# Kernel tuning notes

Hardware: AMD Instinct MI355X
Metric: run time of the kernel (lower is better)

The kernel has to match this reference:

```python
import jax, jax.numpy as jnp
import numpy as np

B, N, D = 16, 1024, 1152
H = 16; DH = D // H
GH = GW = 32; SY = SX = 2
WS = SY * SX                      # tokens per window
NW = (GH // SY) * (GW // SX)      # 256 windows (one dst each)
NS = NW * (WS - 1)                # 768 src tokens
NUM_PRUNE = int(N * 0.5)          # 512
NOISE_ALPHA = 0.1
SIM_BETA = 1.0


def setup_inputs() -> dict:
    key = jax.random.key(0)
    ks = jax.random.split(key, 8)
    rn = lambda k, s: jax.random.normal(k, s, jnp.float32) * 0.02
    return dict(
        x=jax.random.normal(ks[0], (B, N, D), jnp.float32),
        noise=jax.random.uniform(ks[1], (B, NW, WS), jnp.float32),
        ln1_g=jnp.ones((D,), jnp.float32), ln1_b=jnp.zeros((D,), jnp.float32),
        ln2_g=jnp.ones((D,), jnp.float32), ln2_b=jnp.zeros((D,), jnp.float32),
        w_qkv=rn(ks[2], (D, 3 * D)), b_qkv=jnp.zeros((3 * D,), jnp.float32),
        w_proj=rn(ks[3], (D, D)), b_proj=jnp.zeros((D,), jnp.float32),
        w_fc1=rn(ks[4], (D, 4 * D)), b_fc1=jnp.zeros((4 * D,), jnp.float32),
        w_fc2=rn(ks[5], (4 * D, D)), b_fc2=jnp.zeros((D,), jnp.float32),
    )


def _ln(x, g, b):
    mu = x.mean(-1, keepdims=True)
    var = ((x - mu) ** 2).mean(-1, keepdims=True)
    return (x - mu) * jax.lax.rsqrt(var + 1e-6) * g + b


def _dit_block(x, ln1_g, ln1_b, ln2_g, ln2_b, w_qkv, b_qkv, w_proj, b_proj,
               w_fc1, b_fc1, w_fc2, b_fc2):
    Bq, T, _ = x.shape
    y = _ln(x, ln1_g, ln1_b)
    q, k, v = jnp.split(y @ w_qkv + b_qkv, 3, axis=-1)
    hd = lambda t: t.reshape(Bq, T, H, DH).transpose(0, 2, 1, 3)  # [B,H,T,DH]
    q, k, v = hd(q), hd(k), hd(v)
    att = jax.nn.softmax(jnp.einsum('bhqd,bhkd->bhqk', q, k) * (1.0 / np.sqrt(DH)), axis=-1)
    o = jnp.einsum('bhqk,bhkd->bhqd', att, v).transpose(0, 2, 1, 3).reshape(Bq, T, D)
    x = x + o @ w_proj + b_proj
    y = _ln(x, ln2_g, ln2_b)
    return x + jax.nn.gelu(y @ w_fc1 + b_fc1) @ w_fc2 + b_fc2


def _sito_indices(x, noise):
    # SiTo seed (dst) selection + similarity-based prune index computation.
    xn = x / (jnp.linalg.norm(x, axis=-1, keepdims=True) + 1e-6)  # cosine feats
    grid = jnp.arange(N).reshape(GH, GW)
    win = grid.reshape(GH // SY, SY, GW // SX, SX).transpose(0, 2, 1, 3).reshape(NW, WS)
    xw = xn[:, win]                                   # [B,NW,WS,D]
    mean = xw.mean(2, keepdims=True)
    score = SIM_BETA * (xw * mean).sum(-1) + NOISE_ALPHA * noise  # [B,NW,WS]
    dst_local = jnp.argmax(score, axis=-1)            # [B,NW]
    winb = jnp.broadcast_to(win, (B, NW, WS))
    dst_idx = jnp.take_along_axis(winb, dst_local[..., None], -1)[..., 0]  # [B,NW]
    local = jnp.arange(WS)[None, None]
    keymat = jnp.where(local != dst_local[..., None], local, WS)
    src_local = jnp.sort(keymat, -1)[..., : WS - 1]   # non-dst locals, in order
    src_idx = jnp.take_along_axis(winb, src_local, -1).reshape(B, NS)
    a = jnp.take_along_axis(xn, src_idx[..., None], 1)      # [B,NS,D]
    bf = jnp.take_along_axis(xn, dst_idx[..., None], 1)     # [B,NW,D]
    sim = jnp.einsum('bsd,bnd->bsn', a, bf)                 # [B,NS,NW]
    best = jnp.argmax(sim, -1)                              # most-similar dst
    order = jnp.argsort(-jnp.max(sim, -1), axis=-1)
    pruned_pos = order[:, :NUM_PRUNE]
    kept_pos = order[:, NUM_PRUNE:]
    src_kept = jnp.take_along_axis(src_idx, kept_pos, 1)
    src_pruned = jnp.take_along_axis(src_idx, pruned_pos, 1)
    pruned_best = jnp.take_along_axis(best, pruned_pos, 1)
    return dst_idx, src_kept, src_pruned, pruned_best


def reference(x, noise, ln1_g, ln1_b, ln2_g, ln2_b, w_qkv, b_qkv, w_proj, b_proj,
              w_fc1, b_fc1, w_fc2, b_fc2):
    dst_idx, src_kept, src_pruned, pruned_best = _sito_indices(x, noise)
    keep_idx = jnp.concatenate([dst_idx, src_kept], axis=1)          # [B,Nk]
    xk = jnp.take_along_axis(x, keep_idx[..., None], 1)              # prune_fn
    out = _dit_block(xk, ln1_g, ln1_b, ln2_g, ln2_b, w_qkv, b_qkv,
                     w_proj, b_proj, w_fc1, b_fc1, w_fc2, b_fc2)

    def recover_one(o, di, sk, sp, pb):  # recover_fn: scatter + copy-from-dst
        out_dst, out_src = o[:NW], o[NW:]
        full = jnp.zeros((N, D), o.dtype)
        full = full.at[di].set(out_dst)
        full = full.at[sk].set(out_src)
        return full.at[sp].set(out_dst[pb])

    return jax.vmap(recover_one)(out, dst_idx, src_kept, src_pruned, pruned_best)
```

## Files before the change

### kernel.cpp

```cpp
#include <hip/hip_runtime.h>
#include <hip/hip_bf16.h>

namespace {

constexpr int Dd = 1152;

typedef __attribute__((ext_vector_type(8))) short bf16x8;
typedef __attribute__((ext_vector_type(4))) float f32x4;

__device__ __forceinline__ void gload_lds16(const void* g, void* l) {
  __builtin_amdgcn_global_load_lds(
      (const __attribute__((address_space(1))) void*)g,
      (__attribute__((address_space(3))) void*)l, 16, 0, 0);
}

__device__ __forceinline__ float gelu_f(float x) {
  float x3 = x * x * x;
  float z2 = 1.5957691216057308f * (x + 0.044715f * x3);
  float e = __expf(fminf(z2, 30.0f));
  return x * e / (e + 1.0f);
}

__global__ __launch_bounds__(256) void norm_kernel(const float* __restrict__ x,
    float* __restrict__ inv, __hip_bfloat16* __restrict__ xnh,
    __hip_bfloat16* __restrict__ xnl) {
  int row = blockIdx.x * 4 + (threadIdx.x >> 6);
  int lane = threadIdx.x & 63;
  const float2* xr = (const float2*)(x + (size_t)row * Dd);
  float2 v[9];
  float s = 0.f;
  #pragma unroll
  for (int e = 0; e < 9; ++e) {
    v[e] = xr[lane + 64 * e];
    s += v[e].x * v[e].x + v[e].y * v[e].y;
  }
  #pragma unroll
  for (int m = 1; m < 64; m <<= 1) s += __shfl_xor(s, m);
  float iv = 1.0f / (sqrtf(s) + 1e-6f);
  if (lane == 0) inv[row] = iv;
  ushort2* ph = (ushort2*)(xnh + (size_t)row * Dd);
  ushort2* pl = (ushort2*)(xnl + (size_t)row * Dd);
  #pragma unroll
  for (int e = 0; e < 9; ++e) {
    float ax = v[e].x * iv, ay = v[e].y * iv;
    __hip_bfloat16 hx = __float2bfloat16(ax), hy = __float2bfloat16(ay);
    __hip_bfloat16 lx = __float2bfloat16(ax - __bfloat162float(hx));
    __hip_bfloat16 ly = __float2bfloat16(ay - __bfloat162float(hy));
    ph[lane + 64 * e] = make_ushort2(*(ushort*)&hx, *(ushort*)&hy);
    pl[lane + 64 * e] = make_ushort2(*(ushort*)&lx, *(ushort*)&ly);
  }
}

__global__ __launch_bounds__(256) void window_kernel(const float* __restrict__ x,
    const float* __restrict__ inv, const float* __restrict__ noise,
    int* __restrict__ dsti, int* __restrict__ srci) {
  int gidx = blockIdx.x * 4 + (threadIdx.x >> 6);
  int lane = threadIdx.x & 63;
  int b = gidx >> 8, w = gidx & 255;
  int wy = w >> 4, wx = w & 15;
  int t0 = (wy * 2) * 32 + wx * 2;
  int tk[4] = {t0, t0 + 1, t0 + 32, t0 + 33};
  float iv[4]; const float* xr[4];
  #pragma unroll
  for (int j = 0; j < 4; ++j) {
    iv[j] = inv[b * 1024 + tk[j]];
    xr[j] = x + (size_t)(b * 1024 + tk[j]) * Dd;
  }
  float dot[4] = {0.f, 0.f, 0.f, 0.f};
  for (int d = lane; d < Dd; d += 64) {
    float xn[4], sum = 0.f;
    #pragma unroll
    for (int j = 0; j < 4; ++j) { xn[j] = xr[j][d] * iv[j]; sum += xn[j]; }
    #pragma unroll
    for (int j = 0; j < 4; ++j) dot[j] += xn[j] * sum;
  }
  #pragma unroll
  for (int m = 1; m < 64; m <<= 1)
    #pragma unroll
    for (int j = 0; j < 4; ++j) dot[j] += __shfl_xor(dot[j], m);
  if (lane == 0) {
    float best = -1e30f; int bj = 0;
    #pragma unroll
    for (int j = 0; j < 4; ++j) {
      float sc = 0.25f * dot[j] + 0.1f * noise[(size_t)(b * 256 + w) * 4 + j];
      if (sc > best) { best = sc; bj = j; }
    }
    dsti[b * 256 + w] = tk[bj];
    int m = 0;
    #pragma unroll
    for (int j = 0; j < 4; ++j) if (j != bj) srci[b * 768 + w * 3 + (m++)] = tk[j];
  }
}

__global__ __launch_bounds__(256) void simgemm_kernel(
    const __hip_bfloat16* __restrict__ xnh, const __hip_bfloat16* __restrict__ xnl,
    const int* __restrict__ dsti, const int* __restrict__ srci,
    float* __restrict__ mx, int* __restrict__ best) {
  int b = blockIdx.x / 12;
  int m0 = (blockIdx.x % 12) * 64;
  __shared__ __align__(16) __hip_bfloat16 AsH[2][64 * 32];
  __shared__ __align__(16) __hip_bfloat16 AsL[2][64 * 32];
  __shared__ __align__(16) __hip_bfloat16 BsH[2][256 * 32];
  __shared__ __align__(16) __hip_bfloat16 BsL[2][256 * 32];
  const int tid = threadIdx.x, wid = tid >> 6, lane = tid & 63;
  const int g = lane >> 4, lr = lane & 15;

  const int slotRow = tid >> 2;
  const int colByte = (((tid & 3) ^ ((tid >> 3) & 3)) << 4);
  size_t aRow = (size_t)((b << 10) + srci[b * 768 + m0 + slotRow]) * Dd;
  size_t bRow[4];
  #pragma unroll
  for (int p = 0; p < 4; ++p)
    bRow[p] = (size_t)((b << 10) + dsti[b * 256 + p * 64 + slotRow]) * Dd;
  const char* xh = (const char*)xnh;
  const char* xl = (const char*)xnl;

  auto stage = [&](int buf, int k0) {
    size_t ka = (aRow + k0) * 2 + colByte;
    gload_lds16(xh + ka, (char*)AsH + buf * 4096 + wid * 1024);
    gload_lds16(xl + ka, (char*)AsL + buf * 4096 + wid * 1024);
    #pragma unroll
    for (int p = 0; p < 4; ++p) {
      size_t kb = (bRow[p] + k0) * 2 + colByte;
      gload_lds16(xh + kb, (char*)BsH + buf * 16384 + p * 4096 + wid * 1024);
      gload_lds16(xl + kb, (char*)BsL + buf * 16384 + p * 4096 + wid * 1024);
    }
  };

  f32x4 hh[16], hx[16];
  const f32x4 zf = {0.f, 0.f, 0.f, 0.f};
  #pragma unroll
  for (int nf = 0; nf < 16; ++nf) { hh[nf] = zf; hx[nf] = zf; }

  const int roff = ((g ^ ((lr >> 1) & 3)) << 3);
  stage(0, 0);
  asm volatile("s_waitcnt vmcnt(0)" ::: "memory");
  __syncthreads();
  int buf = 0;
  for (int ks = 0; ks < 36; ++ks) {
    if (ks + 1 < 36) stage(buf ^ 1, (ks + 1) * 32);
    bf16x8 ah = *(const bf16x8*)&AsH[buf][(wid * 16 + lr) * 32 + roff];
    bf16x8 al = *(const bf16x8*)&AsL[buf][(wid * 16 + lr) * 32 + roff];
    #pragma unroll
    for (int nf = 0; nf < 16; ++nf) {
      bf16x8 bh = *(const bf16x8*)&BsH[buf][(nf * 16 + lr) * 32 + roff];
      bf16x8 bl = *(const bf16x8*)&BsL[buf][(nf * 16 + lr) * 32 + roff];
      hh[nf] = __builtin_amdgcn_mfma_f32_16x16x32_bf16(ah, bh, hh[nf], 0, 0, 0);
      hx[nf] = __builtin_amdgcn_mfma_f32_16x16x32_bf16(ah, bl, hx[nf], 0, 0, 0);
      hx[nf] = __builtin_amdgcn_mfma_f32_16x16x32_bf16(al, bh, hx[nf], 0, 0, 0);
    }
    asm volatile("s_waitcnt vmcnt(0)" ::: "memory");
    __syncthreads();
    buf ^= 1;
  }

  #pragma unroll
  for (int j = 0; j < 4; ++j) {
    float bv = -1e30f; int bi = 0;
    #pragma unroll
    for (int nf = 0; nf < 16; ++nf) {
      float v = hh[nf][j] + hx[nf][j];
      if (v > bv) { bv = v; bi = nf * 16 + lr; }
    }
    #pragma unroll
    for (int m = 1; m < 16; m <<= 1) {
      float ov = __shfl_xor(bv, m);
      int oi = __shfl_xor(bi, m);
      if (ov > bv || (ov == bv && oi < bi)) { bv = ov; bi = oi; }
    }
    if (lr == 0) {
      int row = m0 + wid * 16 + g * 4 + j;
      mx[b * 768 + row] = bv;
      best[b * 768 + row] = bi;
    }
  }
}

__global__ __launch_bounds__(256) void rank_kernel(const float* __restrict__ mx,
    const int* __restrict__ best, const int* __restrict__ dsti,
    const int* __restrict__ srci, int* __restrict__ keep, int* __restrict__ srow) {
  int b = blockIdx.x;
  int tid = threadIdx.x;
  __shared__ float smx[768];
  for (int i = tid; i < 768; i += 256) smx[i] = mx[b * 768 + i];
  __syncthreads();
  if (tid < 256) {
    int t = dsti[b * 256 + tid];
    keep[b * 512 + tid] = t;
    srow[b * 1024 + t] = tid;
  }
  for (int i = tid; i < 768; i += 256) {
    float v = smx[i];
    int r = 0;
    for (int s = 0; s < 768; ++s) {
      float u = smx[s];
      r += (u > v) || (u == v && s < i);
    }
    int tok = srci[b * 768 + i];
    if (r >= 512) {
      keep[b * 512 + (r - 256)] = tok;
      srow[b * 1024 + tok] = r - 256;
    } else {
      srow[b * 1024 + tok] = best[b * 768 + i];
    }
  }
}

template<int GATHER>
__global__ __launch_bounds__(256) void ln_kernel(const float* __restrict__ xin,
    const int* __restrict__ keep, const float* __restrict__ gw,
    const float* __restrict__ bw, __hip_bfloat16* __restrict__ yout) {
  int row = blockIdx.x;
  const float* xr;
  if (GATHER) {
    int b = row >> 9, t = row & 511;
    int tok = keep[(b << 9) + t];
    xr = xin + (size_t)((b << 10) + tok) * Dd;
  } else {
    xr = xin + (size_t)row * Dd;
  }
  int tid = threadIdx.x;
  float v[5];
  float s = 0.f, s2 = 0.f;
  #pragma unroll
  for (int e = 0; e < 5; ++e) {
    int i = tid + e * 256;
    float val = (i < Dd) ? xr[i] : 0.f;
    v[e] = val; s += val; s2 += val * val;
  }
  #pragma unroll
  for (int m = 1; m < 64; m <<= 1) { s += __shfl_xor(s, m); s2 += __shfl_xor(s2, m); }
  __shared__ float ps[4], ps2[4];
  int wid = tid >> 6, lane = tid & 63;
  if (lane == 0) { ps[wid] = s; ps2[wid] = s2; }
  __syncthreads();
  s = ps[0] + ps[1] + ps[2] + ps[3];
  s2 = ps2[0] + ps2[1] + ps2[2] + ps2[3];
  constexpr float inv_d = 1.0f / Dd;
  float mu = s * inv_d;
  float var = s2 * inv_d - mu * mu;
  float rstd = rsqrtf(var + 1e-6f);
  __hip_bfloat16* yr = yout + (size_t)row * Dd;
  #pragma unroll
  for (int e = 0; e < 5; ++e) {
    int i = tid + e * 256;
    if (i < Dd) {
      yr[i] = __float2bfloat16((v[e] - mu) * rstd * gw[i] + bw[i]);
    }
  }
}

__global__ __launch_bounds__(256) void wtrans_kernel(const float* __restrict__ w,
    __hip_bfloat16* __restrict__ wT, int K, int N) {
  __shared__ float tile[32][33];
  int nt = N >> 5;
  int tk = blockIdx.x / nt, tn = blockIdx.x % nt;
  int tid = threadIdx.x;
  #pragma unroll
  for (int e = 0; e < 4; ++e) {
    int idx = tid + e * 256;
    int r = idx >> 5, c = idx & 31;
    tile[r][c] = w[(size_t)(tk * 32 + r) * N + tn * 32 + c];
  }
  __syncthreads();
  #pragma unroll
  for (int e = 0; e < 4; ++e) {
    int idx = tid + e * 256;
    int r = idx >> 5, c = idx & 31;
    wT[(size_t)(tn * 32 + r) * K + tk * 32 + c] = __float2bfloat16(tile[c][r]);
  }
}

template<int EPI>
__device__ __forceinline__ void epi_store(void* C, const float* res, int Nd,
                                          size_t row, size_t col, float v) {
  if (EPI == 0) {
    ((__hip_bfloat16*)C)[row * (size_t)Nd + col] = __float2bfloat16(v);
  } else if (EPI == 1) {
    ((float*)C)[row * (size_t)Nd + col] = v + res[row * (size_t)Nd + col];
  } else if (EPI == 2) {
    ((__hip_bfloat16*)C)[row * (size_t)Nd + col] = __float2bfloat16(gelu_f(v));
  }
}

template<int EPI>
__global__ __launch_bounds__(512, 4) void gemm128_kernel(
    const __hip_bfloat16* __restrict__ A, const __hip_bfloat16* __restrict__ BT,
    const float* __restrict__ bias, const float* __restrict__ res,
    const int* __restrict__ keepIdx, const float* __restrict__ xsrc,
    void* __restrict__ C, int Md, int Nd, int NdPad, int Kd) {
  constexpr int BM = 128;
  __shared__ __align__(16) __hip_bfloat16 As[3][BM * 32];
  __shared__ __align__(16) __hip_bfloat16 Bs[3][256 * 32];
  const int nb = NdPad >> 8;
  const int q8 = gridDim.x >> 3;
  const int wg = (blockIdx.x & 7) * q8 + (blockIdx.x >> 3);
  const int bm = wg / nb, bnb = wg % nb;
  const int tid = threadIdx.x, wid = tid >> 6, lane = tid & 63;
  const int g = lane >> 4, lr = lane & 15;
  const int wm = wid >> 2, wn = wid & 3;
  const size_t m0 = (size_t)bm * BM, n0 = (size_t)bnb * 256;

  const int trow = tid >> 2;
  const int scol = (((tid & 3) ^ ((tid >> 3) & 3)) << 3);
  const char* Ab = (const char*)A;
  const char* Bb = (const char*)BT;

  auto stage = [&](int slot, int kt) {
    const size_t kb = ((size_t)kt << 5) + scol;
    gload_lds16(Ab + (((m0 + trow) * (size_t)Kd + kb) << 1),
                (char*)As + slot * 8192 + wid * 1024);
    gload_lds16(Bb + (((n0 + trow) * (size_t)Kd + kb) << 1),
                (char*)Bs + slot * 16384 + wid * 1024);
    gload_lds16(Bb + (((n0 + 128 + trow) * (size_t)Kd + kb) << 1),
                (char*)Bs + slot * 16384 + 8192 + wid * 1024);
  };

  f32x4 acc[4][4];
  const f32x4 zf = {0.f, 0.f, 0.f, 0.f};
  #pragma unroll
  for (int mi = 0; mi < 4; ++mi)
    #pragma unroll
    for (int ni = 0; ni < 4; ++ni) acc[mi][ni] = zf;

  const int nk = Kd >> 5;
  stage(0, 0);
  stage(1, 1);
  asm volatile("s_waitcnt vmcnt(3)" ::: "memory");
  __builtin_amdgcn_s_barrier();

  int cur = 0;
  const int roff = ((g ^ ((lr >> 1) & 3)) << 3);
  for (int kt = 0; kt < nk; ++kt) {
    const __hip_bfloat16* Ac = As[cur];
    const __hip_bfloat16* Bc = Bs[cur];
    bf16x8 af[4], bf[4];
    #pragma unroll
    for (int mi = 0; mi < 4; ++mi)
      af[mi] = *(const bf16x8*)&Ac[(wm * 64 + mi * 16 + lr) * 32 + roff];
    #pragma unroll
    for (int ni = 0; ni < 4; ++ni)
      bf[ni] = *(const bf16x8*)&Bc[(wn * 64 + ni * 16 + lr) * 32 + roff];
    if (kt + 2 < nk) stage(cur == 0 ? 2 : cur - 1, kt + 2);
    __builtin_amdgcn_s_barrier();
    __builtin_amdgcn_s_setprio(1);
    #pragma unroll
    for (int mi = 0; mi < 4; ++mi)
      #pragma unroll
      for (int ni = 0; ni < 4; ++ni)
        acc[mi][ni] = __builtin_amdgcn_mfma_f32_16x16x32_bf16(af[mi], bf[ni], acc[mi][ni], 0, 0, 0);
    __builtin_amdgcn_s_setprio(0);
    if (kt + 2 < nk)      asm volatile("s_waitcnt vmcnt(3)" ::: "memory");
    else if (kt + 1 < nk) asm volatile("s_waitcnt vmcnt(0)" ::: "memory");
    __builtin_amdgcn_s_barrier();
    cur = (cur == 2) ? 0 : cur + 1;
  }

  #pragma unroll
  for (int ni = 0; ni < 4; ++ni) {
    size_t col = n0 + wn * 64 + ni * 16 + lr;
    if (col < (size_t)Nd) {
      float bv = bias[col];
      #pragma unroll
      for (int mi = 0; mi < 4; ++mi) {
        #pragma unroll
        for (int j = 0; j < 4; ++j) {
          size_t row = m0 + wm * 64 + mi * 16 + g * 4 + j;
          float v = acc[mi][ni][j] + bv;
          if (EPI == 3) {
            int b = (int)(row >> 9);
            int tok = keepIdx[row];
            const float* rr = xsrc + ((size_t)(b << 10) + tok) * Dd;
            ((float*)C)[row * (size_t)Nd + col] = v + rr[col];
          } else {
            epi_store<EPI>(C, res, Nd, row, col, v);
          }
        }
      }
    }
  }
}

__global__ __launch_bounds__(256) void vtrans_kernel(const __hip_bfloat16* __restrict__ qkv,
                                                     __hip_bfloat16* __restrict__ vT) {
  int bh = blockIdx.x;
  int b = bh >> 4, h = bh & 15;
  __shared__ __align__(16) __hip_bfloat16 Vl[256 * 72];
  int tid = threadIdx.x;
  const __hip_bfloat16 zb = __float2bfloat16(0.0f);
  for (int half = 0; half < 2; ++half) {
    __syncthreads();
    for (int idx = tid; idx < 256 * 18; idx += 256) {
      int t = idx / 18, c = idx % 18;
      *(ushort4*)&Vl[t * 72 + c * 4] =
          *(const ushort4*)&qkv[((size_t)(b * 512 + half * 256 + t)) * 3456 + 2304 + h * 72 + c * 4];
    }
    __syncthreads();
    for (int idx = tid; idx < 80 * 256; idx += 256) {
      int d = idx >> 8, t = idx & 255;
      vT[((size_t)bh * 80 + d) * 512 + half * 256 + t] = (d < 72) ? Vl[t * 72 + d] : zb;
    }
  }
}

__global__ __launch_bounds__(256) void attn_kernel(const __hip_bfloat16* __restrict__ qkv,
    const __hip_bfloat16* __restrict__ vT, __hip_bfloat16* __restrict__ o) {
  const int blk = blockIdx.x;
  const int qt = blk & 7, bh = blk >> 3;
  const int b = bh >> 4, h = bh & 15;
  __shared__ __align__(16) __hip_bfloat16 Qs[64][96];
  __shared__ __align__(16) __hip_bfloat16 Ks[64][96];
  __shared__ __align__(16) __hip_bfloat16 Vs[80][72];
  __shared__ __align__(16) __hip_bfloat16 Ps[4][16][72];
  const int tid = threadIdx.x, wid = tid >> 6, lane = tid & 63;
  const int g = lane >> 4, lr = lane & 15;
  const __hip_bfloat16 zb = __float2bfloat16(0.0f);

  for (int idx = tid; idx < 64 * 18; idx += 256) {
    int r = idx / 18, c = idx % 18;
    *(ushort4*)&Qs[r][c * 4] =
        *(const ushort4*)&qkv[((size_t)(b * 512 + qt * 64 + r)) * 3456 + h * 72 + c * 4];
  }
  for (int idx = tid; idx < 64 * 24; idx += 256) {
    int r = idx / 24, d = 72 + idx % 24;
    Qs[r][d] = zb; Ks[r][d] = zb;
  }

  f32x4 ov[5];
  const f32x4 zf = {0.f, 0.f, 0.f, 0.f};
  #pragma unroll
  for (int ni = 0; ni < 5; ++ni) ov[ni] = zf;
  float m_[4], l_[4];
  #pragma unroll
  for (int j = 0; j < 4; ++j) { m_[j] = -3.0e38f; l_[j] = 0.f; }
  const float scale = 0.11785113019775793f;

  for (int c = 0; c < 8; ++c) {
    __syncthreads();
    for (int idx = tid; idx < 64 * 18; idx += 256) {
      int r = idx / 18, cc = idx % 18;
      *(ushort4*)&Ks[r][cc * 4] =
          *(const ushort4*)&qkv[((size_t)(b * 512 + c * 64 + r)) * 3456 + 1152 + h * 72 + cc * 4];
    }
    for (int idx = tid; idx < 80 * 8; idx += 256) {
      int d = idx >> 3, t8 = idx & 7;
      *(uint4*)&Vs[d][t8 * 8] =
          *(const uint4*)&vT[((size_t)bh * 80 + d) * 512 + c * 64 + t8 * 8];
    }
    __syncthreads();

    f32x4 sf[4];
    #pragma unroll
    for (int nf = 0; nf < 4; ++nf) sf[nf] = zf;
    #pragma unroll
    for (int ks = 0; ks < 3; ++ks) {
      bf16x8 qa = *(const bf16x8*)&Qs[wid * 16 + lr][ks * 32 + g * 8];
      #pragma unroll
      for (int nf = 0; nf < 4; ++nf) {
        bf16x8 kb = *(const bf16x8*)&Ks[nf * 16 + lr][ks * 32 + g * 8];
        sf[nf] = __builtin_amdgcn_mfma_f32_16x16x32_bf16(qa, kb, sf[nf], 0, 0, 0);
      }
    }

    float cm[4];
    #pragma unroll
    for (int j = 0; j < 4; ++j)
      cm[j] = fmaxf(fmaxf(sf[0][j], sf[1][j]), fmaxf(sf[2][j], sf[3][j])) * scale;
    #pragma unroll
    for (int mm = 1; mm < 16; mm <<= 1)
      #pragma unroll
      for (int j = 0; j < 4; ++j) cm[j] = fmaxf(cm[j], __shfl_xor(cm[j], mm));
    float fac[4], rs[4];
    #pragma unroll
    for (int j = 0; j < 4; ++j) {
      float nm = fmaxf(m_[j], cm[j]);
      fac[j] = __expf(m_[j] - nm);
      m_[j] = nm;
      rs[j] = 0.f;
    }
    #pragma unroll
    for (int nf = 0; nf < 4; ++nf)
      #pragma unroll
      for (int j = 0; j < 4; ++j) {
        float pv = __expf(sf[nf][j] * scale - m_[j]);
        rs[j] += pv;
        Ps[wid][g * 4 + j][nf * 16 + lr] = __float2bfloat16(pv);
      }
    #pragma unroll
    for (int mm = 1; mm < 16; mm <<= 1)
      #pragma unroll
      for (int j = 0; j < 4; ++j) rs[j] += __shfl_xor(rs[j], mm);
    #pragma unroll
    for (int j = 0; j < 4; ++j) l_[j] = l_[j] * fac[j] + rs[j];
    #pragma unroll
    for (int ni = 0; ni < 5; ++ni)
      #pragma unroll
      for (int j = 0; j < 4; ++j) ov[ni][j] *= fac[j];

    #pragma unroll
    for (int k2 = 0; k2 < 2; ++k2) {
      bf16x8 pa = *(const bf16x8*)&Ps[wid][lr][k2 * 32 + g * 8];
      #pragma unroll
      for (int ni = 0; ni < 5; ++ni) {
        bf16x8 vb = *(const bf16x8*)&Vs[ni * 16 + lr][k2 * 32 + g * 8];
        ov[ni] = __builtin_amdgcn_mfma_f32_16x16x32_bf16(pa, vb, ov[ni], 0, 0, 0);
      }
    }
  }

  #pragma unroll
  for (int ni = 0; ni < 5; ++ni) {
    int d = ni * 16 + lr;
    if (d < 72) {
      #pragma unroll
      for (int j = 0; j < 4; ++j) {
        int t = qt * 64 + wid * 16 + g * 4 + j;
        o[((size_t)(b * 512 + t)) * 1152 + h * 72 + d] = __float2bfloat16(ov[ni][j] / l_[j]);
      }
    }
  }
}

__global__ __launch_bounds__(256) void recover_kernel(const float* __restrict__ yout,
    const int* __restrict__ srow, float* __restrict__ out) {
  int idx = blockIdx.x * 256 + threadIdx.x;
  int q = idx % 288;
  int bnv = idx / 288;
  int r = srow[bnv];
  int b = bnv >> 10;
  const float4* src = (const float4*)yout + ((size_t)((b << 9) + r)) * 288 + q;
  ((float4*)out)[idx] = *src;
}

}

extern "C" void kernel_launch(void* const* d_in, const int* in_sizes, int n_in,
                              void* d_out, int out_size, void* d_ws, size_t ws_size,
                              hipStream_t stream) {
  (void)in_sizes; (void)n_in; (void)out_size; (void)ws_size;
  const float* x      = (const float*)d_in[0];
  const float* noise  = (const float*)d_in[1];
  const float* ln1_g  = (const float*)d_in[2];
  const float* ln1_b  = (const float*)d_in[3];
  const float* ln2_g  = (const float*)d_in[4];
  const float* ln2_b  = (const float*)d_in[5];
  const float* w_qkv  = (const float*)d_in[6];
  const float* b_qkv  = (const float*)d_in[7];
  const float* w_proj = (const float*)d_in[8];
  const float* b_proj = (const float*)d_in[9];
  const float* w_fc1  = (const float*)d_in[10];
  const float* b_fc1  = (const float*)d_in[11];
  const float* w_fc2  = (const float*)d_in[12];
  const float* b_fc2  = (const float*)d_in[13];
  float* out = (float*)d_out;

  char* p = (char*)d_ws;
  auto alloc = [&](size_t bytes) {
    char* r = p;
    p += (bytes + 255) & ~(size_t)255;
    return r;
  };
  __hip_bfloat16* wqkvT  = (__hip_bfloat16*)alloc((size_t)3584 * 1152 * 2);
  __hip_bfloat16* wprojT = (__hip_bfloat16*)alloc((size_t)1280 * 1152 * 2);
  __hip_bfloat16* wfc1T  = (__hip_bfloat16*)alloc((size_t)4608 * 1152 * 2);
  __hip_bfloat16* wfc2T  = (__hip_bfloat16*)alloc((size_t)1280 * 4608 * 2);
  float* inv = (float*)alloc(16384 * 4);
  int* dsti  = (int*)alloc(4096 * 4);
  int* srci  = (int*)alloc(12288 * 4);
  float* mx  = (float*)alloc(12288 * 4);
  int* best  = (int*)alloc(12288 * 4);
  int* keep  = (int*)alloc(8192 * 4);
  int* srow  = (int*)alloc(16384 * 4);
  float* yout = (float*)alloc((size_t)8192 * 1152 * 4);
  __hip_bfloat16* y1   = (__hip_bfloat16*)alloc((size_t)8192 * 1152 * 2);
  __hip_bfloat16* qkvb = (__hip_bfloat16*)alloc((size_t)8192 * 4608 * 2);
  __hip_bfloat16* vT   = (__hip_bfloat16*)alloc((size_t)256 * 80 * 512 * 2);
  __hip_bfloat16* ob   = (__hip_bfloat16*)alloc((size_t)8192 * 1152 * 2);
  float* x2 = (float*)alloc((size_t)8192 * 1152 * 4);

  __hip_bfloat16* xnh = qkvb;
  __hip_bfloat16* xnl = qkvb + (size_t)16 * 1024 * 1152;

  wtrans_kernel<<<36 * 108, 256, 0, stream>>>(w_qkv, wqkvT, 1152, 3456);
  wtrans_kernel<<<36 * 36, 256, 0, stream>>>(w_proj, wprojT, 1152, 1152);
  wtrans_kernel<<<36 * 144, 256, 0, stream>>>(w_fc1, wfc1T, 1152, 4608);
  wtrans_kernel<<<144 * 36, 256, 0, stream>>>(w_fc2, wfc2T, 4608, 1152);

  norm_kernel<<<4096, 256, 0, stream>>>(x, inv, xnh, xnl);
  window_kernel<<<1024, 256, 0, stream>>>(x, inv, noise, dsti, srci);
  simgemm_kernel<<<16 * 12, 256, 0, stream>>>(xnh, xnl, dsti, srci, mx, best);
  rank_kernel<<<16, 256, 0, stream>>>(mx, best, dsti, srci, keep, srow);

  ln_kernel<1><<<8192, 256, 0, stream>>>(x, keep, ln1_g, ln1_b, y1);
  gemm128_kernel<0><<<64 * 14, 512, 0, stream>>>(y1, wqkvT, b_qkv, nullptr, nullptr, nullptr,
                                                 qkvb, 8192, 3456, 3584, 1152);
  vtrans_kernel<<<256, 256, 0, stream>>>(qkvb, vT);
  attn_kernel<<<2048, 256, 0, stream>>>(qkvb, vT, ob);
  gemm128_kernel<3><<<64 * 5, 512, 0, stream>>>(ob, wprojT, b_proj, nullptr, keep, x,
                                                x2, 8192, 1152, 1280, 1152);
  ln_kernel<0><<<8192, 256, 0, stream>>>(x2, nullptr, ln2_g, ln2_b, y1);
  gemm128_kernel<2><<<64 * 18, 512, 0, stream>>>(y1, wfc1T, b_fc1, nullptr, nullptr, nullptr,
                                                 qkvb, 8192, 4608, 4608, 1152);
  gemm128_kernel<1><<<64 * 5, 512, 0, stream>>>(qkvb, wfc2T, b_fc2, x2, nullptr, nullptr,
                                                yout, 8192, 1152, 1280, 4608);

  recover_kernel<<<18432, 256, 0, stream>>>(yout, srow, out);
}
```

Baseline: 769.4 us.

## Fuse norm and window scoring; add 128x128 triple-buffered GEMM for proj/MLP

Merges the row-normalization and window seed-selection kernels into one, where each block handles a 2x2 window and shares the normalized rows through LDS instead of re-reading x from global memory. Adds a new 128x128-tile, 256-thread GEMM with a three-stage LDS pipeline and XCD-aware block remapping, and uses it for the projection, fc1 and fc2 GEMMs in place of the older 512-thread kernel. The new tiling removes the padded N (1280 to 1152) and aims for higher occupancy, at the cost of smaller per-block work and a different load/MFMA schedule.

Result: faster. 735.7 us (-4.4%).

```diff
diff --git a/kernel.cpp b/kernel.cpp
--- a/kernel.cpp
+++ b/kernel.cpp
@@ -21,11 +21,18 @@
   return x * e / (e + 1.0f);
 }
 
-__global__ __launch_bounds__(256) void norm_kernel(const float* __restrict__ x,
-    float* __restrict__ inv, __hip_bfloat16* __restrict__ xnh,
-    __hip_bfloat16* __restrict__ xnl) {
-  int row = blockIdx.x * 4 + (threadIdx.x >> 6);
-  int lane = threadIdx.x & 63;
+__global__ __launch_bounds__(256) void normwin_kernel(const float* __restrict__ x,
+    const float* __restrict__ noise, float* __restrict__ inv,
+    __hip_bfloat16* __restrict__ xnh, __hip_bfloat16* __restrict__ xnl,
+    int* __restrict__ dsti, int* __restrict__ srci) {
+  const int gidx = blockIdx.x;
+  const int b = gidx >> 8, w = gidx & 255;
+  const int wy = w >> 4, wx = w & 15;
+  const int t0 = wy * 64 + wx * 2;
+  const int wid = threadIdx.x >> 6, lane = threadIdx.x & 63;
+  const int tok = t0 + (wid >> 1) * 32 + (wid & 1);
+  const int row = (b << 10) + tok;
+
   const float2* xr = (const float2*)(x + (size_t)row * Dd);
   float2 v[9];
   float s = 0.f;
@@ -38,53 +45,44 @@
   for (int m = 1; m < 64; m <<= 1) s += __shfl_xor(s, m);
   float iv = 1.0f / (sqrtf(s) + 1e-6f);
   if (lane == 0) inv[row] = iv;
+
+  __shared__ float2 xns[4][576];
   ushort2* ph = (ushort2*)(xnh + (size_t)row * Dd);
   ushort2* pl = (ushort2*)(xnl + (size_t)row * Dd);
   #pragma unroll
   for (int e = 0; e < 9; ++e) {
     float ax = v[e].x * iv, ay = v[e].y * iv;
+    xns[wid][lane + 64 * e] = make_float2(ax, ay);
     __hip_bfloat16 hx = __float2bfloat16(ax), hy = __float2bfloat16(ay);
     __hip_bfloat16 lx = __float2bfloat16(ax - __bfloat162float(hx));
     __hip_bfloat16 ly = __float2bfloat16(ay - __bfloat162float(hy));
     ph[lane + 64 * e] = make_ushort2(*(ushort*)&hx, *(ushort*)&hy);
     pl[lane + 64 * e] = make_ushort2(*(ushort*)&lx, *(ushort*)&ly);
   }
-}
-
-__global__ __launch_bounds__(256) void window_kernel(const float* __restrict__ x,
-    const float* __restrict__ inv, const float* __restrict__ noise,
-    int* __restrict__ dsti, int* __restrict__ srci) {
-  int gidx = blockIdx.x * 4 + (threadIdx.x >> 6);
-  int lane = threadIdx.x & 63;
-  int b = gidx >> 8, w = gidx & 255;
-  int wy = w >> 4, wx = w & 15;
-  int t0 = (wy * 2) * 32 + wx * 2;
-  int tk[4] = {t0, t0 + 1, t0 + 32, t0 + 33};
-  float iv[4]; const float* xr[4];
-  #pragma unroll
-  for (int j = 0; j < 4; ++j) {
-    iv[j] = inv[b * 1024 + tk[j]];
-    xr[j] = x + (size_t)(b * 1024 + tk[j]) * Dd;
-  }
-  float dot[4] = {0.f, 0.f, 0.f, 0.f};
-  for (int d = lane; d < Dd; d += 64) {
-    float xn[4], sum = 0.f;
-    #pragma unroll
-    for (int j = 0; j < 4; ++j) { xn[j] = xr[j][d] * iv[j]; sum += xn[j]; }
-    #pragma unroll
-    for (int j = 0; j < 4; ++j) dot[j] += xn[j] * sum;
-  }
-  #pragma unroll
-  for (int m = 1; m < 64; m <<= 1)
-    #pragma unroll
-    for (int j = 0; j < 4; ++j) dot[j] += __shfl_xor(dot[j], m);
-  if (lane == 0) {
+  __syncthreads();
+
+  float dot = 0.f;
+  #pragma unroll
+  for (int e = 0; e < 9; ++e) {
+    int i = lane + 64 * e;
+    float2 a0 = xns[0][i], a1 = xns[1][i], a2 = xns[2][i], a3 = xns[3][i];
+    float sx = a0.x + a1.x + a2.x + a3.x;
+    float sy = a0.y + a1.y + a2.y + a3.y;
+    dot += (v[e].x * iv) * sx + (v[e].y * iv) * sy;
+  }
+  #pragma unroll
+  for (int m = 1; m < 64; m <<= 1) dot += __shfl_xor(dot, m);
+  __shared__ float dots[4];
+  if (lane == 0) dots[wid] = dot;
+  __syncthreads();
+  if (threadIdx.x == 0) {
     float best = -1e30f; int bj = 0;
     #pragma unroll
     for (int j = 0; j < 4; ++j) {
-      float sc = 0.25f * dot[j] + 0.1f * noise[(size_t)(b * 256 + w) * 4 + j];
+      float sc = 0.25f * dots[j] + 0.1f * noise[(size_t)gidx * 4 + j];
       if (sc > best) { best = sc; bj = j; }
     }
+    int tk[4] = {t0, t0 + 1, t0 + 32, t0 + 33};
     dsti[b * 256 + w] = tk[bj];
     int m = 0;
     #pragma unroll
@@ -375,6 +373,103 @@
           } else {
             epi_store<EPI>(C, res, Nd, row, col, v);
           }
+        }
+      }
+    }
+  }
+}
+
+template<int EPI>
+__global__ __launch_bounds__(256, 3) void gemm128n_kernel(
+    const __hip_bfloat16* __restrict__ A, const __hip_bfloat16* __restrict__ BT,
+    const float* __restrict__ bias, const float* __restrict__ res,
+    const int* __restrict__ keepIdx, const float* __restrict__ xsrc,
+    void* __restrict__ C, int Md, int Nd, int Kd) {
+  __shared__ __align__(16) __hip_bfloat16 As[3][128 * 32];
+  __shared__ __align__(16) __hip_bfloat16 Bs[3][128 * 32];
+  const int nb = Nd >> 7;
+  const int q8 = gridDim.x >> 3;
+  const int wg = (blockIdx.x & 7) * q8 + (blockIdx.x >> 3);
+  const int bm = wg / nb, bnb = wg % nb;
+  const int tid = threadIdx.x, wid = tid >> 6, lane = tid & 63;
+  const int g = lane >> 4, lr = lane & 15;
+  const int wm = wid >> 1, wn = wid & 1;
+  const size_t m0 = (size_t)bm * 128, n0 = (size_t)bnb * 128;
+
+  const int trow = tid >> 2;
+  const int scol = (((tid & 3) ^ ((tid >> 3) & 3)) << 3);
+  const char* Ab = (const char*)A;
+  const char* Bb = (const char*)BT;
+
+  auto stage = [&](int slot, int kt) {
+    const size_t kb = ((size_t)kt << 5) + scol;
+    #pragma unroll
+    for (int c = 0; c < 2; ++c)
+      gload_lds16(Ab + (((m0 + c * 64 + trow) * (size_t)Kd + kb) << 1),
+                  (char*)As + slot * 8192 + c * 4096 + tid * 16);
+    #pragma unroll
+    for (int c = 0; c < 2; ++c)
+      gload_lds16(Bb + (((n0 + c * 64 + trow) * (size_t)Kd + kb) << 1),
+                  (char*)Bs + slot * 8192 + c * 4096 + tid * 16);
+  };
+
+  f32x4 acc[4][4];
+  const f32x4 zf = {0.f, 0.f, 0.f, 0.f};
+  #pragma unroll
+  for (int mi = 0; mi < 4; ++mi)
+    #pragma unroll
+    for (int ni = 0; ni < 4; ++ni) acc[mi][ni] = zf;
+
+  const int nk = Kd >> 5;
+  stage(0, 0);
+  stage(1, 1);
+  asm volatile("s_waitcnt vmcnt(4)" ::: "memory");
+  __builtin_amdgcn_s_barrier();
+
+  int cur = 0;
+  const int roff = ((g ^ ((lr >> 1) & 3)) << 3);
+  for (int kt = 0; kt < nk; ++kt) {
+    const __hip_bfloat16* Ac = As[cur];
+    const __hip_bfloat16* Bc = Bs[cur];
+    bf16x8 af[4], bf[4];
+    #pragma unroll
+    for (int mi = 0; mi < 4; ++mi)
+      af[mi] = *(const bf16x8*)&Ac[(wm * 64 + mi * 16 + lr) * 32 + roff];
+    #pragma unroll
+    for (int ni = 0; ni < 4; ++ni)
+      bf[ni] = *(const bf16x8*)&Bc[(wn * 64 + ni * 16 + lr) * 32 + roff];
+    if (kt + 2 < nk) stage(cur == 0 ? 2 : cur - 1, kt + 2);
+    __builtin_amdgcn_s_barrier();
+    __builtin_amdgcn_s_setprio(1);
+    #pragma unroll
+    for (int mi = 0; mi < 4; ++mi)
+      #pragma unroll
+      for (int ni = 0; ni < 4; ++ni)
+        acc[mi][ni] = __builtin_amdgcn_mfma_f32_16x16x32_bf16(af[mi], bf[ni], acc[mi][ni], 0, 0, 0);
+    __builtin_amdgcn_s_setprio(0);
+    if (kt + 2 < nk)      asm volatile("s_waitcnt vmcnt(4)" ::: "memory");
+    else if (kt + 1 < nk) asm volatile("s_waitcnt vmcnt(0)" ::: "memory");
+    __builtin_amdgcn_s_barrier();
+    cur = (cur == 2) ? 0 : cur + 1;
+  }
+
+  #pragma unroll
+  for (int ni = 0; ni < 4; ++ni) {
+    size_t col = n0 + wn * 64 + ni * 16 + lr;
+    float bv = bias[col];
+    #pragma unroll
+    for (int mi = 0; mi < 4; ++mi) {
+      #pragma unroll
+      for (int j = 0; j < 4; ++j) {
+        size_t row = m0 + wm * 64 + mi * 16 + g * 4 + j;
+        float v = acc[mi][ni][j] + bv;
+        if (EPI == 3) {
+          int b = (int)(row >> 9);
+          int tok = keepIdx[row];
+          const float* rr = xsrc + ((size_t)(b << 10) + tok) * Dd;
+          ((float*)C)[row * (size_t)Nd + col] = v + rr[col];
+        } else {
+          epi_store<EPI>(C, res, Nd, row, col, v);
         }
       }
     }
@@ -586,8 +681,7 @@
   wtrans_kernel<<<36 * 144, 256, 0, stream>>>(w_fc1, wfc1T, 1152, 4608);
   wtrans_kernel<<<144 * 36, 256, 0, stream>>>(w_fc2, wfc2T, 4608, 1152);
 
-  norm_kernel<<<4096, 256, 0, stream>>>(x, inv, xnh, xnl);
-  window_kernel<<<1024, 256, 0, stream>>>(x, inv, noise, dsti, srci);
+  normwin_kernel<<<4096, 256, 0, stream>>>(x, noise, inv, xnh, xnl, dsti, srci);
   simgemm_kernel<<<16 * 12, 256, 0, stream>>>(xnh, xnl, dsti, srci, mx, best);
   rank_kernel<<<16, 256, 0, stream>>>(mx, best, dsti, srci, keep, srow);
 
@@ -596,13 +690,13 @@
                                                  qkvb, 8192, 3456, 3584, 1152);
   vtrans_kernel<<<256, 256, 0, stream>>>(qkvb, vT);
   attn_kernel<<<2048, 256, 0, stream>>>(qkvb, vT, ob);
-  gemm128_kernel<3><<<64 * 5, 512, 0, stream>>>(ob, wprojT, b_proj, nullptr, keep, x,
-                                                x2, 8192, 1152, 1280, 1152);
+  gemm128n_kernel<3><<<64 * 9, 256, 0, stream>>>(ob, wprojT, b_proj, nullptr, keep, x,
+                                                 x2, 8192, 1152, 1152);
   ln_kernel<0><<<8192, 256, 0, stream>>>(x2, nullptr, ln2_g, ln2_b, y1);
-  gemm128_kernel<2><<<64 * 18, 512, 0, stream>>>(y1, wfc1T, b_fc1, nullptr, nullptr, nullptr,
-                                                 qkvb, 8192, 4608, 4608, 1152);
-  gemm128_kernel<1><<<64 * 5, 512, 0, stream>>>(qkvb, wfc2T, b_fc2, x2, nullptr, nullptr,
-                                                yout, 8192, 1152, 1280, 4608);
+  gemm128n_kernel<2><<<64 * 36, 256, 0, stream>>>(y1, wfc1T, b_fc1, nullptr, nullptr, nullptr,
+                                                  qkvb, 8192, 4608, 1152);
+  gemm128n_kernel<1><<<64 * 9, 256, 0, stream>>>(qkvb, wfc2T, b_fc2, x2, nullptr, nullptr,
+                                                 yout, 8192, 1152, 4608);
 
   recover_kernel<<<18432, 256, 0, stream>>>(yout, srow, out);
 }
```
